# Optimization experiments

Measured on AMD Instinct MI355X. Metric: run time of the kernel, lower is better.

Reference implementation:

```python
import jax, jax.numpy as jnp
import numpy as np

EMBED_DIM = 1024
NUM_HEADS = 16
HEAD_DIM = EMBED_DIM // NUM_HEADS
LN_EPS = 1e-5


def setup_inputs() -> dict:
    key = jax.random.key(0)
    ks = jax.random.split(key, 7)
    B, N, D = 4, 2048, EMBED_DIM
    s = 1.0 / np.sqrt(D)  # ~kaiming-uniform scale for Linear weights
    return {
        "inputs": jax.random.normal(ks[0], (B, N, D), dtype=jnp.float32),
        "W_q": jax.random.uniform(ks[1], (D, D), jnp.float32, -s, s),
        "W_k": jax.random.uniform(ks[2], (D, D), jnp.float32, -s, s),
        "W_v": jax.random.uniform(ks[3], (D, D), jnp.float32, -s, s),
        "W_o": jax.random.uniform(ks[4], (D, D), jnp.float32, -s, s),
        "ln_gamma": jnp.ones((D,), jnp.float32),
        "ln_beta": jnp.zeros((D,), jnp.float32),
    }


def reference(inputs, W_q, W_k, W_v, W_o, ln_gamma, ln_beta):
    x = inputs
    B, N, D = x.shape
    H, Hd = NUM_HEADS, HEAD_DIM
    # torch nn.Linear computes x @ W.T; W_* stored as (out, in)
    q = (x @ W_q.T).reshape(B, N, H, Hd).transpose(0, 2, 1, 3)  # [B,H,N,Hd]
    k = (x @ W_k.T).reshape(B, N, H, Hd).transpose(0, 2, 1, 3)
    v = (x @ W_v.T).reshape(B, N, H, Hd).transpose(0, 2, 1, 3)
    scores = jnp.einsum("bhqd,bhkd->bhqk", q, k) / jnp.sqrt(jnp.float32(Hd))
    attn = jax.nn.softmax(scores, axis=-1)  # dropout p=0 -> identity
    out = jnp.einsum("bhqk,bhkd->bhqd", attn, v)
    out = out.transpose(0, 2, 1, 3).reshape(B, N, D)
    out = out @ W_o.T
    # residual + LayerNorm
    y = out + x
    mu = jnp.mean(y, axis=-1, keepdims=True)
    var = jnp.mean(jnp.square(y - mu), axis=-1, keepdims=True)
    y = (y - mu) * jax.lax.rsqrt(var + LN_EPS)
    return y * ln_gamma + ln_beta
```

## Files before the change

kernel.cpp:

```cpp
#include <hip/hip_runtime.h>
#include <hip/hip_bf16.h>
#include <stdint.h>

typedef __attribute__((ext_vector_type(8))) short bf16x8;
typedef __attribute__((ext_vector_type(4))) float f32x4;

#define GLOBAL_AS __attribute__((address_space(1)))
#define LDS_AS    __attribute__((address_space(3)))

__device__ __forceinline__ void load_lds16(const void* g, void* l) {
  __builtin_amdgcn_global_load_lds((const GLOBAL_AS void*)g, (LDS_AS void*)l, 16, 0, 0);
}

__device__ __forceinline__ short f2bfn(float f) {
  __hip_bfloat16 h = __float2bfloat16(f);
  return __builtin_bit_cast(short, h);
}
__device__ __forceinline__ float bf2f(short s) {
  return __uint_as_float(((unsigned)(unsigned short)s) << 16);
}

__global__ __launch_bounds__(256) void cvt_all(const float* __restrict__ x,
                                               const float* __restrict__ q,
                                               const float* __restrict__ k,
                                               const float* __restrict__ v,
                                               const float* __restrict__ o,
                                               short* __restrict__ xb,
                                               short* __restrict__ Wb,
                                               short* __restrict__ Wob) {
  const int bid = blockIdx.x;
  const float* src;
  short* dst;
  int i;
  if (bid < 4096) {
    src = x; dst = xb; i = (bid * 256 + threadIdx.x) * 8;
  } else {
    const int sel = (bid - 4096) >> 9;
    const int inner = (bid - 4096) & 511;
    i = (inner * 256 + threadIdx.x) * 8;
    src = sel == 0 ? q : sel == 1 ? k : sel == 2 ? v : o;
    dst = sel == 0 ? Wb : sel == 1 ? Wb + 1024 * 1024
        : sel == 2 ? Wb + 2 * 1024 * 1024 : Wob;
  }
  float4 a = *(const float4*)(src + i);
  float4 b = *(const float4*)(src + i + 4);
  bf16x8 ov;
  ov[0] = f2bfn(a.x); ov[1] = f2bfn(a.y); ov[2] = f2bfn(a.z); ov[3] = f2bfn(a.w);
  ov[4] = f2bfn(b.x); ov[5] = f2bfn(b.y); ov[6] = f2bfn(b.z); ov[7] = f2bfn(b.w);
  *(bf16x8*)(dst + i) = ov;
}

__global__ __launch_bounds__(512, 2) void gemm8_qk(const short* __restrict__ xb,
                                                   const short* __restrict__ Wqk,
                                                   short* __restrict__ qkv) {
  __shared__ short As[2][256 * 64];
  __shared__ short Bs[2][256 * 64];
  const int t = threadIdx.x, l = t & 63, w = t >> 6;
  const int g = l >> 4, li = l & 15, sw = li & 7;
  const int wm = w >> 2, wn = w & 3;
  const int bid = blockIdx.x;
  const int work = (bid & 7) * 32 + (bid >> 3);
  const int bm = work >> 3, bn = work & 7;
  const int K = 1024;
  const size_t arow0 = (size_t)(bm * 256) * K;
  const size_t brow0 = (size_t)(bn * 256) * K;
  f32x4 acc[8][4] = {};

#define STAGE8(buf, k0_)                                                        \
  {                                                                             \
    _Pragma("unroll")                                                           \
    for (int it = 0; it < 4; ++it) {                                            \
      int e = it * 4096 + t * 8;                                                \
      int r = e >> 6;                                                           \
      int cg = (t & 7) ^ (r & 7);                                               \
      load_lds16(xb + arow0 + (size_t)r * K + ((k0_) + cg * 8), &As[buf][e]);   \
      load_lds16(Wqk + brow0 + (size_t)r * K + ((k0_) + cg * 8), &Bs[buf][e]);  \
    }                                                                           \
  }

  STAGE8(0, 0);
  for (int kt = 0; kt < 16; ++kt) {
    const int cur = kt & 1;
    if (kt < 15) {
      STAGE8(cur ^ 1, (kt + 1) * 64);
      asm volatile("s_waitcnt vmcnt(8)" ::: "memory");
    } else {
      asm volatile("s_waitcnt vmcnt(0)" ::: "memory");
    }
    __syncthreads();

    bf16x8 afc[4][2];
    bf16x8 bfc[4][2];
#pragma unroll
    for (int ph = 0; ph < 4; ++ph) {
      const int mh = ph >> 1, nh = ph & 1;
      if (nh == 0) {
#pragma unroll
        for (int m = 0; m < 4; ++m)
#pragma unroll
          for (int kk = 0; kk < 2; ++kk)
            afc[m][kk] = *(const bf16x8*)&As[cur][(wm * 128 + (mh * 4 + m) * 16 + li) * 64 +
                                                 (((kk * 4 + g) ^ sw) * 8)];
      }
      if (ph < 2) {
#pragma unroll
        for (int n2 = 0; n2 < 2; ++n2)
#pragma unroll
          for (int kk = 0; kk < 2; ++kk)
            bfc[ph * 2 + n2][kk] = *(const bf16x8*)&Bs[cur][(wn * 64 + (ph * 2 + n2) * 16 + li) * 64 +
                                                           (((kk * 4 + g) ^ sw) * 8)];
      }
      __syncthreads();
      __builtin_amdgcn_s_setprio(1);
#pragma unroll
      for (int m = 0; m < 4; ++m)
#pragma unroll
        for (int n2 = 0; n2 < 2; ++n2)
#pragma unroll
          for (int kk = 0; kk < 2; ++kk) {
            const int mi = mh * 4 + m, ni = nh * 2 + n2;
            acc[mi][ni] = __builtin_amdgcn_mfma_f32_16x16x32_bf16(afc[m][kk], bfc[ni][kk],
                                                                  acc[mi][ni], 0, 0, 0);
          }
      __builtin_amdgcn_s_setprio(0);
      __syncthreads();
    }
  }
#undef STAGE8

#pragma unroll
  for (int m = 0; m < 8; ++m)
#pragma unroll
    for (int n = 0; n < 4; ++n)
#pragma unroll
      for (int r = 0; r < 4; ++r) {
        int row = bm * 256 + wm * 128 + m * 16 + g * 4 + r;
        int col = bn * 256 + wn * 64 + n * 16 + li;
        qkv[(size_t)row * 3072 + col] = f2bfn(acc[m][n][r]);
      }
}

__global__ __launch_bounds__(256) void gemm_vt(const short* __restrict__ Wv,
                                               const short* __restrict__ xb,
                                               short* __restrict__ VT) {
  __shared__ short As[128 * 64];
  __shared__ short Bs[128 * 64];
  const int t = threadIdx.x, l = t & 63, w = t >> 6;
  const int g = l >> 4, li = l & 15;
  const int wr = w >> 1, wc = w & 1;
  const int bid = blockIdx.x;
  const int bm = bid & 7;
  const int bn = bid >> 3;
  const int sw = li & 7;
  const int K = 1024;
  f32x4 acc[4][4] = {};
  const size_t arow0 = (size_t)(bm * 128) * K;
  const size_t brow0 = (size_t)(bn * 128) * K;
  for (int k0 = 0; k0 < K; k0 += 64) {
    __syncthreads();
#pragma unroll
    for (int it = 0; it < 4; ++it) {
      int e = it * 2048 + t * 8;
      int r = e >> 6;
      int cs = (e >> 3) & 7;
      int cg = cs ^ (r & 7);
      load_lds16(Wv + arow0 + (size_t)r * K + (k0 + cg * 8), &As[e]);
      load_lds16(xb + brow0 + (size_t)r * K + (k0 + cg * 8), &Bs[e]);
    }
    __syncthreads();
#pragma unroll
    for (int kk = 0; kk < 2; ++kk) {
      bf16x8 af[4], bfr[4];
#pragma unroll
      for (int m = 0; m < 4; ++m)
        af[m] = *(const bf16x8*)&As[(wr * 64 + m * 16 + li) * 64 + (((kk * 4 + g) ^ sw) * 8)];
#pragma unroll
      for (int n = 0; n < 4; ++n)
        bfr[n] = *(const bf16x8*)&Bs[(wc * 64 + n * 16 + li) * 64 + (((kk * 4 + g) ^ sw) * 8)];
#pragma unroll
      for (int m = 0; m < 4; ++m)
#pragma unroll
        for (int n = 0; n < 4; ++n)
          acc[m][n] = __builtin_amdgcn_mfma_f32_16x16x32_bf16(af[m], bfr[n], acc[m][n], 0, 0, 0);
    }
  }
#pragma unroll
  for (int m = 0; m < 4; ++m)
#pragma unroll
    for (int n = 0; n < 4; ++n)
#pragma unroll
      for (int r = 0; r < 4; ++r) {
        int row = bm * 128 + wr * 64 + m * 16 + g * 4 + r;
        int col = bn * 128 + wc * 64 + n * 16 + li;
        VT[(size_t)(col >> 11) * (1024 * 2048) + (size_t)row * 2048 +
           (col & 2047)] = f2bfn(acc[m][n][r]);
      }
}

__global__ __launch_bounds__(256) void gemm_projres(const short* __restrict__ A,
                                                    const short* __restrict__ B,
                                                    const short* __restrict__ xb,
                                                    short* __restrict__ Up) {
  __shared__ short As[128 * 64];
  __shared__ short Bs[128 * 64];
  const int t = threadIdx.x, l = t & 63, w = t >> 6;
  const int g = l >> 4, li = l & 15;
  const int wr = w >> 1, wc = w & 1;
  const int bid = blockIdx.x;
  const int bm = (bid & 7) * 8 + ((bid >> 3) & 7);
  const int bn = bid >> 6;
  const int sw = li & 7;
  const int K = 1024;
  f32x4 acc[4][4] = {};
  const size_t arow0 = (size_t)(bm * 128) * K;
  const size_t brow0 = (size_t)(bn * 128) * K;
  for (int k0 = 0; k0 < K; k0 += 64) {
    __syncthreads();
#pragma unroll
    for (int it = 0; it < 4; ++it) {
      int e = it * 2048 + t * 8;
      int r = e >> 6;
      int cs = (e >> 3) & 7;
      int cg = cs ^ (r & 7);
      load_lds16(A + arow0 + (size_t)r * K + (k0 + cg * 8), &As[e]);
      load_lds16(B + brow0 + (size_t)r * K + (k0 + cg * 8), &Bs[e]);
    }
    __syncthreads();
#pragma unroll
    for (int kk = 0; kk < 2; ++kk) {
      bf16x8 af[4], bfr[4];
#pragma unroll
      for (int m = 0; m < 4; ++m)
        af[m] = *(const bf16x8*)&As[(wr * 64 + m * 16 + li) * 64 + (((kk * 4 + g) ^ sw) * 8)];
#pragma unroll
      for (int n = 0; n < 4; ++n)
        bfr[n] = *(const bf16x8*)&Bs[(wc * 64 + n * 16 + li) * 64 + (((kk * 4 + g) ^ sw) * 8)];
#pragma unroll
      for (int m = 0; m < 4; ++m)
#pragma unroll
        for (int n = 0; n < 4; ++n)
          acc[m][n] = __builtin_amdgcn_mfma_f32_16x16x32_bf16(af[m], bfr[n], acc[m][n], 0, 0, 0);
    }
  }
#pragma unroll
  for (int m = 0; m < 4; ++m)
#pragma unroll
    for (int n = 0; n < 4; ++n)
#pragma unroll
      for (int r = 0; r < 4; ++r) {
        int row = bm * 128 + wr * 64 + m * 16 + g * 4 + r;
        int col = bn * 128 + wc * 64 + n * 16 + li;
        float v = acc[m][n][r] + bf2f(xb[(size_t)row * 1024 + col]);
        Up[(size_t)row * 1024 + col] = f2bfn(v);
      }
}

__global__ __launch_bounds__(512, 4) void attn_fwd(const short* __restrict__ qkv,
                                                   const short* __restrict__ VT,
                                                   short* __restrict__ obuf) {
  const int f0 = blockIdx.x;
  const int work = (f0 & 7) * 64 + (f0 >> 3);
  const int qt = work & 7;
  const int bh = work >> 3;
  const int b = bh >> 4, h = bh & 15;
  const int t = threadIdx.x, w = t >> 6, l = t & 63;
  const int g = l >> 4, li = l & 15;

  __shared__ short Ks[2][64 * 64];
  __shared__ short Vts[2][64 * 64];
  __shared__ short Ps[8][2][16 * 64];

  const size_t base = (size_t)b * 2048 * 3072 + (size_t)h * 64;
  const short* Vsrc = VT + (size_t)bh * 64 * 2048;

  bf16x8 qf[2][2];
  {
    const float QSC = 0.125f * 1.44269504088896341f;
#pragma unroll
    for (int qh = 0; qh < 2; ++qh) {
      const short* qp = qkv + base + (size_t)(qt * 256 + w * 32 + qh * 16 + li) * 3072;
#pragma unroll
      for (int c = 0; c < 2; ++c) {
        bf16x8 v = *(const bf16x8*)(qp + c * 32 + g * 8);
#pragma unroll
        for (int i = 0; i < 8; ++i) {
          float f = bf2f(v[i]);
          v[i] = f2bfn(f * QSC);
        }
        qf[qh][c] = v;
      }
    }
  }

  bf16x8 ones;
#pragma unroll
  for (int i = 0; i < 8; ++i) ones[i] = (short)0x3F80;
  const f32x4 fz = {0.f, 0.f, 0.f, 0.f};

  f32x4 o_[2][4], lacc[2];
#pragma unroll
  for (int qh = 0; qh < 2; ++qh) {
#pragma unroll
    for (int dj = 0; dj < 4; ++dj) o_[qh][dj] = (f32x4){0.f, 0.f, 0.f, 0.f};
    lacc[qh] = (f32x4){0.f, 0.f, 0.f, 0.f};
  }

  const int sw = li & 7;

#define STAGE(buf, kt_)                                                          \
  {                                                                              \
    int e = t * 8;                                                               \
    int r = e >> 6;                                                              \
    int cs = (e >> 3) & 7;                                                       \
    int cg = cs ^ (r & 7);                                                       \
    load_lds16(qkv + base + 1024 + (size_t)((kt_) * 64 + r) * 3072 + cg * 8,     \
               &Ks[buf][e]);                                                     \
    load_lds16(Vsrc + (size_t)r * 2048 + (kt_) * 64 + cg * 8, &Vts[buf][e]);     \
  }

  STAGE(0, 0);
  asm volatile("s_waitcnt vmcnt(0)" ::: "memory");
  __syncthreads();

  for (int kt = 0; kt < 32; ++kt) {
    const int cur = kt & 1;
    if (kt + 1 < 32) STAGE(cur ^ 1, kt + 1);

    f32x4 s_[2][4];
    __builtin_amdgcn_s_setprio(1);
#pragma unroll
    for (int j = 0; j < 4; ++j) {
      bf16x8 kf = *(const bf16x8*)&Ks[cur][(j * 16 + li) * 64 + ((g ^ sw) * 8)];
      s_[0][j] = __builtin_amdgcn_mfma_f32_16x16x32_bf16(kf, qf[0][0], fz, 0, 0, 0);
      s_[1][j] = __builtin_amdgcn_mfma_f32_16x16x32_bf16(kf, qf[1][0], fz, 0, 0, 0);
    }
#pragma unroll
    for (int j = 0; j < 4; ++j) {
      bf16x8 kf = *(const bf16x8*)&Ks[cur][(j * 16 + li) * 64 + ((((4 + g)) ^ sw) * 8)];
      s_[0][j] = __builtin_amdgcn_mfma_f32_16x16x32_bf16(kf, qf[0][1], s_[0][j], 0, 0, 0);
      s_[1][j] = __builtin_amdgcn_mfma_f32_16x16x32_bf16(kf, qf[1][1], s_[1][j], 0, 0, 0);
    }
    __builtin_amdgcn_s_setprio(0);

#pragma unroll
    for (int qh = 0; qh < 2; ++qh) {
#pragma unroll
      for (int j = 0; j < 4; ++j) {
        float p0 = exp2f(s_[qh][j][0]);
        float p1 = exp2f(s_[qh][j][1]);
        float p2 = exp2f(s_[qh][j][2]);
        float p3 = exp2f(s_[qh][j][3]);
        unsigned u0, u1;
        asm("v_cvt_pk_bf16_f32 %0, %1, %2" : "=v"(u0) : "v"(p0), "v"(p1));
        asm("v_cvt_pk_bf16_f32 %0, %1, %2" : "=v"(u1) : "v"(p2), "v"(p3));
        uint2 pk2; pk2.x = u0; pk2.y = u1;
        int pos = (j * 16 + g * 4) ^ (sw << 3);
        *(uint2*)&Ps[w][qh][li * 64 + pos] = pk2;
      }
    }
    asm volatile("s_waitcnt lgkmcnt(0)" ::: "memory");

    __builtin_amdgcn_s_setprio(1);
#pragma unroll
    for (int c = 0; c < 2; ++c) {
      bf16x8 vb[4];
#pragma unroll
      for (int dj = 0; dj < 4; ++dj)
        vb[dj] = *(const bf16x8*)&Vts[cur][(dj * 16 + li) * 64 + (((c * 4 + g) ^ sw) * 8)];
#pragma unroll
      for (int qh = 0; qh < 2; ++qh) {
        bf16x8 pa = *(const bf16x8*)&Ps[w][qh][li * 64 + (((c * 4 + g) ^ sw) * 8)];
        lacc[qh] = __builtin_amdgcn_mfma_f32_16x16x32_bf16(pa, ones, lacc[qh], 0, 0, 0);
#pragma unroll
        for (int dj = 0; dj < 4; ++dj)
          o_[qh][dj] = __builtin_amdgcn_mfma_f32_16x16x32_bf16(pa, vb[dj], o_[qh][dj], 0, 0, 0);
      }
    }
    __builtin_amdgcn_s_setprio(0);

    asm volatile("s_waitcnt vmcnt(0)" ::: "memory");
    __syncthreads();
  }

#pragma unroll
  for (int qh = 0; qh < 2; ++qh)
#pragma unroll
    for (int r = 0; r < 4; ++r) {
      float ilr = 1.f / lacc[qh][r];
      int row = b * 2048 + qt * 256 + w * 32 + qh * 16 + g * 4 + r;
#pragma unroll
      for (int dj = 0; dj < 4; ++dj) {
        int col = h * 64 + dj * 16 + li;
        obuf[(size_t)row * 1024 + col] = f2bfn(o_[qh][dj][r] * ilr);
      }
    }
#undef STAGE
}

__global__ __launch_bounds__(256) void resid_ln(const short* __restrict__ Up,
                                                const float* __restrict__ gamma,
                                                const float* __restrict__ beta,
                                                float* __restrict__ out) {
  const int t = threadIdx.x, w = t >> 6, l = t & 63;
  __shared__ float red[4];
  const float4 gg = *(const float4*)(gamma + t * 4);
  const float4 bb = *(const float4*)(beta + t * 4);
  for (int rr = 0; rr < 4; ++rr) {
    const int row = blockIdx.x * 4 + rr;
    short4 uv = *(const short4*)(Up + (size_t)row * 1024 + t * 4);
    float y[4] = {bf2f(uv.x), bf2f(uv.y), bf2f(uv.z), bf2f(uv.w)};
    float s = (y[0] + y[1]) + (y[2] + y[3]);
#pragma unroll
    for (int d = 1; d < 64; d <<= 1) s += __shfl_xor(s, d);
    if (l == 0) red[w] = s;
    __syncthreads();
    s = red[0] + red[1] + red[2] + red[3];
    const float mu = s * (1.f / 1024.f);
    float vs = 0.f;
#pragma unroll
    for (int i = 0; i < 4; ++i) { float d0 = y[i] - mu; vs += d0 * d0; }
#pragma unroll
    for (int d = 1; d < 64; d <<= 1) vs += __shfl_xor(vs, d);
    __syncthreads();
    if (l == 0) red[w] = vs;
    __syncthreads();
    vs = red[0] + red[1] + red[2] + red[3];
    const float rstd = rsqrtf(vs * (1.f / 1024.f) + 1e-5f);
    float4 oo;
    oo.x = (y[0] - mu) * rstd * gg.x + bb.x;
    oo.y = (y[1] - mu) * rstd * gg.y + bb.y;
    oo.z = (y[2] - mu) * rstd * gg.z + bb.z;
    oo.w = (y[3] - mu) * rstd * gg.w + bb.w;
    *(float4*)(out + (size_t)row * 1024 + t * 4) = oo;
    __syncthreads();
  }
}

extern "C" void kernel_launch(void* const* d_in, const int* in_sizes, int n_in,
                              void* d_out, int out_size, void* d_ws, size_t ws_size,
                              hipStream_t stream) {
  const float* x     = (const float*)d_in[0];
  const float* W_q   = (const float*)d_in[1];
  const float* W_k   = (const float*)d_in[2];
  const float* W_v   = (const float*)d_in[3];
  const float* W_o   = (const float*)d_in[4];
  const float* gamma = (const float*)d_in[5];
  const float* beta  = (const float*)d_in[6];
  float* out = (float*)d_out;

  char* ws = (char*)d_ws;
  short* xb   = (short*)ws;  ws += (size_t)8192 * 1024 * 2;
  short* Wb   = (short*)ws;  ws += (size_t)3072 * 1024 * 2;
  short* Wob  = (short*)ws;  ws += (size_t)1024 * 1024 * 2;
  short* qkv  = (short*)ws;  ws += (size_t)8192 * 3072 * 2;
  short* obuf = (short*)ws;  ws += (size_t)8192 * 1024 * 2;
  short* Up   = (short*)ws;  ws += (size_t)8192 * 1024 * 2;
  short* VT   = (short*)ws;  ws += (size_t)64 * 64 * 2048 * 2;

  cvt_all<<<6144, 256, 0, stream>>>(x, W_q, W_k, W_v, W_o, xb, Wb, Wob);
  gemm8_qk<<<256, 512, 0, stream>>>(xb, Wb, qkv);
  gemm_vt<<<512, 256, 0, stream>>>(Wb + 2 * 1024 * 1024, xb, VT);
  attn_fwd<<<512, 512, 0, stream>>>(qkv, VT, obuf);
  gemm_projres<<<512, 256, 0, stream>>>(obuf, Wob, xb, Up);
  resid_ln<<<2048, 256, 0, stream>>>(Up, gamma, beta, out);
}
```

Before: 214.1 us.

## Merge V-transpose GEMM into the QK GEMM kernel as extra tiles

Drops the separate 128x128-tile gemm_vt kernel and adds its work as 128 extra 256x256 tiles in the double-buffered 512-thread QK GEMM kernel. The grid grows from 256 to 384 blocks, and a per-block branch picks the operands and the output layout (row-major qkv or transposed VT). The intent is to remove one launch and the tail between kernels, and to run the V projection on the faster pipelined tile path. In exchange there is a branch in the epilogue, and 384 blocks may fill the CUs unevenly.

```diff
diff --git a/kernel.cpp b/kernel.cpp
--- a/kernel.cpp
+++ b/kernel.cpp
@@ -50,17 +50,30 @@
   *(bf16x8*)(dst + i) = ov;
 }
 
-__global__ __launch_bounds__(512, 2) void gemm8_qk(const short* __restrict__ xb,
-                                                   const short* __restrict__ Wqk,
-                                                   short* __restrict__ qkv) {
+__global__ __launch_bounds__(512, 2) void gemm8_qkvt(const short* __restrict__ xb,
+                                                     const short* __restrict__ Wqk,
+                                                     const short* __restrict__ Wv,
+                                                     short* __restrict__ qkv,
+                                                     short* __restrict__ VT) {
   __shared__ short As[2][256 * 64];
   __shared__ short Bs[2][256 * 64];
   const int t = threadIdx.x, l = t & 63, w = t >> 6;
   const int g = l >> 4, li = l & 15, sw = li & 7;
   const int wm = w >> 2, wn = w & 3;
   const int bid = blockIdx.x;
-  const int work = (bid & 7) * 32 + (bid >> 3);
-  const int bm = work >> 3, bn = work & 7;
+  const int work = (bid & 7) * 48 + (bid >> 3);
+  const bool isqk = work < 256;
+  const short* A;
+  const short* B;
+  int bm, bn;
+  if (isqk) {
+    A = xb; B = Wqk;
+    bm = work >> 3; bn = work & 7;
+  } else {
+    const int w2 = work - 256;
+    A = Wv; B = xb;
+    bm = w2 >> 5; bn = w2 & 31;
+  }
   const int K = 1024;
   const size_t arow0 = (size_t)(bm * 256) * K;
   const size_t brow0 = (size_t)(bn * 256) * K;
@@ -73,8 +86,8 @@
       int e = it * 4096 + t * 8;                                                \
       int r = e >> 6;                                                           \
       int cg = (t & 7) ^ (r & 7);                                               \
-      load_lds16(xb + arow0 + (size_t)r * K + ((k0_) + cg * 8), &As[buf][e]);   \
-      load_lds16(Wqk + brow0 + (size_t)r * K + ((k0_) + cg * 8), &Bs[buf][e]);  \
+      load_lds16(A + arow0 + (size_t)r * K + ((k0_) + cg * 8), &As[buf][e]);    \
+      load_lds16(B + brow0 + (size_t)r * K + ((k0_) + cg * 8), &Bs[buf][e]);    \
     }                                                                           \
   }
 
@@ -136,64 +149,11 @@
       for (int r = 0; r < 4; ++r) {
         int row = bm * 256 + wm * 128 + m * 16 + g * 4 + r;
         int col = bn * 256 + wn * 64 + n * 16 + li;
-        qkv[(size_t)row * 3072 + col] = f2bfn(acc[m][n][r]);
-      }
-}
-
-__global__ __launch_bounds__(256) void gemm_vt(const short* __restrict__ Wv,
-                                               const short* __restrict__ xb,
-                                               short* __restrict__ VT) {
-  __shared__ short As[128 * 64];
-  __shared__ short Bs[128 * 64];
-  const int t = threadIdx.x, l = t & 63, w = t >> 6;
-  const int g = l >> 4, li = l & 15;
-  const int wr = w >> 1, wc = w & 1;
-  const int bid = blockIdx.x;
-  const int bm = bid & 7;
-  const int bn = bid >> 3;
-  const int sw = li & 7;
-  const int K = 1024;
-  f32x4 acc[4][4] = {};
-  const size_t arow0 = (size_t)(bm * 128) * K;
-  const size_t brow0 = (size_t)(bn * 128) * K;
-  for (int k0 = 0; k0 < K; k0 += 64) {
-    __syncthreads();
-#pragma unroll
-    for (int it = 0; it < 4; ++it) {
-      int e = it * 2048 + t * 8;
-      int r = e >> 6;
-      int cs = (e >> 3) & 7;
-      int cg = cs ^ (r & 7);
-      load_lds16(Wv + arow0 + (size_t)r * K + (k0 + cg * 8), &As[e]);
-      load_lds16(xb + brow0 + (size_t)r * K + (k0 + cg * 8), &Bs[e]);
-    }
-    __syncthreads();
-#pragma unroll
-    for (int kk = 0; kk < 2; ++kk) {
-      bf16x8 af[4], bfr[4];
-#pragma unroll
-      for (int m = 0; m < 4; ++m)
-        af[m] = *(const bf16x8*)&As[(wr * 64 + m * 16 + li) * 64 + (((kk * 4 + g) ^ sw) * 8)];
-#pragma unroll
-      for (int n = 0; n < 4; ++n)
-        bfr[n] = *(const bf16x8*)&Bs[(wc * 64 + n * 16 + li) * 64 + (((kk * 4 + g) ^ sw) * 8)];
-#pragma unroll
-      for (int m = 0; m < 4; ++m)
-#pragma unroll
-        for (int n = 0; n < 4; ++n)
-          acc[m][n] = __builtin_amdgcn_mfma_f32_16x16x32_bf16(af[m], bfr[n], acc[m][n], 0, 0, 0);
-    }
-  }
-#pragma unroll
-  for (int m = 0; m < 4; ++m)
-#pragma unroll
-    for (int n = 0; n < 4; ++n)
-#pragma unroll
-      for (int r = 0; r < 4; ++r) {
-        int row = bm * 128 + wr * 64 + m * 16 + g * 4 + r;
-        int col = bn * 128 + wc * 64 + n * 16 + li;
-        VT[(size_t)(col >> 11) * (1024 * 2048) + (size_t)row * 2048 +
-           (col & 2047)] = f2bfn(acc[m][n][r]);
+        if (isqk)
+          qkv[(size_t)row * 3072 + col] = f2bfn(acc[m][n][r]);
+        else
+          VT[(size_t)(col >> 11) * (1024 * 2048) + (size_t)row * 2048 +
+             (col & 2047)] = f2bfn(acc[m][n][r]);
       }
 }
 
@@ -458,8 +418,7 @@
   short* VT   = (short*)ws;  ws += (size_t)64 * 64 * 2048 * 2;
 
   cvt_all<<<6144, 256, 0, stream>>>(x, W_q, W_k, W_v, W_o, xb, Wb, Wob);
-  gemm8_qk<<<256, 512, 0, stream>>>(xb, Wb, qkv);
-  gemm_vt<<<512, 256, 0, stream>>>(Wb + 2 * 1024 * 1024, xb, VT);
+  gemm8_qkvt<<<384, 512, 0, stream>>>(xb, Wb, Wb + 2 * 1024 * 1024, qkv, VT);
   attn_fwd<<<512, 512, 0, stream>>>(qkv, VT, obuf);
   gemm_projres<<<512, 256, 0, stream>>>(obuf, Wob, xb, Up);
   resid_ln<<<2048, 256, 0, stream>>>(Up, gamma, beta, out);
```

Measured after the change: 231.6 us. 8.2% more time.
